# Kernel optimization log

Measured on AMD Instinct MI355X. Metric: run time of the kernel, lower is better.

The kernel has to match this reference:

```python
import jax, jax.numpy as jnp
import numpy as np

B, N = 8, 2048
D_IN, D_FEAT, H, K = 2, 30, 64, 8
D_ATT = D_IN + D_FEAT + H  # 96, per-head attention input dim
ALPHA = 0.2
NEG = -1e9


def setup_inputs() -> dict:
    key = jax.random.key(0)
    ks = jax.random.split(key, 11)
    inputs = jax.random.normal(ks[0], (B, N, D_IN), jnp.float32)
    envs_feat = jax.random.normal(ks[1], (B, N, D_FEAT), jnp.float32)
    state_t = jax.random.normal(ks[2], (B, N, H), jnp.float32)
    conn = jax.random.uniform(ks[3], (N, N)) < 0.05
    conn = conn | jnp.eye(N, dtype=bool)
    bias_mat = jnp.where(conn, 0.0, NEG).astype(jnp.float32)
    # xavier-ish init (gain 1.414)
    def xav(k, shape, fi, fo):
        lim = 1.414 * np.sqrt(6.0 / (fi + fo))
        return jax.random.uniform(k, shape, jnp.float32, -lim, lim)
    W_h = xav(ks[4], (K, D_ATT, H), D_ATT, H)      # stacked per-head W
    a1_h = xav(ks[5], (K, H), H, 1)
    a2_h = xav(ks[6], (K, H), H, 1)
    W_o = xav(ks[7], (K * H, H), K * H, H)
    a1_o = xav(ks[8], (H,), H, 1)
    a2_o = xav(ks[9], (H,), H, 1)
    return {"inputs": inputs, "envs_feat": envs_feat, "state_t": state_t,
            "bias_mat": bias_mat, "W_h": W_h, "a1_h": a1_h, "a2_h": a2_h,
            "W_o": W_o, "a1_o": a1_o, "a2_o": a2_o}


def _gat_multihead(h, bias, W, a1, a2):
    # h: [b,n,d], W: [k,d,h], a1/a2: [k,h], bias: [n,n]
    Wh = jnp.einsum('bnd,kdh->bknh', h, W)
    f1 = jnp.einsum('bknh,kh->bkn', Wh, a1)
    f2 = jnp.einsum('bknh,kh->bkn', Wh, a2)
    e = jax.nn.leaky_relu(f1[:, :, :, None] + f2[:, :, None, :], ALPHA) + bias  # [b,k,n,n]
    att = jax.nn.softmax(e, axis=-1)
    return jnp.einsum('bknm,bkmh->bknh', att, Wh)  # [b,k,n,h]


def _gat_single(h, bias, W, a1, a2):
    # h: [b,n,d], W: [d,h], a1/a2: [h]
    Wh = jnp.einsum('bnd,dh->bnh', h, W)
    f1 = Wh @ a1  # [b,n]
    f2 = Wh @ a2
    e = jax.nn.leaky_relu(f1[:, :, None] + f2[:, None, :], ALPHA) + bias  # [b,n,n]
    att = jax.nn.softmax(e, axis=-1)
    return jnp.einsum('bnm,bmh->bnh', att, Wh)


def reference(inputs, envs_feat, state_t, bias_mat, W_h, a1_h, a2_h, W_o, a1_o, a2_o):
    b, n = inputs.shape[0], inputs.shape[1]
    h = jnp.concatenate([inputs, envs_feat, state_t], axis=2)  # [b,n,D_ATT]
    hp = _gat_multihead(h, bias_mat, W_h, a1_h, a2_h)          # [b,k,n,h]
    h1 = jax.nn.elu(hp)
    h1 = jnp.transpose(h1, (0, 2, 1, 3)).reshape(b, n, -1)     # concat heads: [b,n,k*h]
    out = jax.nn.elu(_gat_single(h1, bias_mat, W_o, a1_o, a2_o))
    return out
```

## Files before the change

### kernel.cpp

```cpp
#include <hip/hip_runtime.h>
#include <hip/hip_bf16.h>
#include <math.h>

#define B   8
#define N   2048
#define DIN 2
#define DF  30
#define HH  64
#define KK  8
#define DATT 96
#define CAP 384
#define CAPL 176
#define ALPHA 0.2f

__device__ __forceinline__ float lrelu(float x) { return x > 0.f ? x : ALPHA * x; }
__device__ __forceinline__ float elu1(float x)  { return x > 0.f ? x : (__expf(x) - 1.f); }
__device__ __forceinline__ unsigned short f2bf(float x) {
    __hip_bfloat16 h = __float2bfloat16(x);
    return *reinterpret_cast<unsigned short*>(&h);
}

__global__ void k_mask(const float* __restrict__ bias, int* __restrict__ cols,
                       int* __restrict__ cnt) {
    int i = blockIdx.x;
    int lane = threadIdx.x;
    int c = 0;
    for (int j0 = 0; j0 < N; j0 += 64) {
        float v = bias[(size_t)i * N + j0 + lane];
        bool conn = v > -1e8f;
        unsigned long long m = __ballot(conn);
        if (conn) {
            int pos = c + __popcll(m & ((1ull << lane) - 1ull));
            if (pos < CAP) cols[i * CAP + pos] = j0 + lane;
        }
        c += __popcll(m);
    }
    if (lane == 0) cnt[i] = c < CAP ? c : CAP;
}

__global__ void k_wh(const float* __restrict__ inp, const float* __restrict__ envs,
                     const float* __restrict__ st,  const float* __restrict__ W_h,
                     const float* __restrict__ a1,  const float* __restrict__ a2,
                     __hip_bfloat16* __restrict__ Whb,
                     float* __restrict__ f1, float* __restrict__ f2) {
    __shared__ float Ws[DATT * HH];
    __shared__ float hs[16 * 98];
    int k = blockIdx.y, b = blockIdx.z;
    int i0 = blockIdx.x * 16;
    int tid = threadIdx.x, lane = tid & 63, w = tid >> 6;
    int g = lane >> 4, sub = lane & 15;
    int r = w * 4 + g;

    const float* Wk = W_h + k * DATT * HH;
    for (int idx = tid * 4; idx < DATT * HH; idx += 1024)
        *(float4*)&Ws[idx] = *(const float4*)&Wk[idx];
    {
        int row = tid >> 4, q = tid & 15;
        float4 v = *(const float4*)&st[(size_t)(b * N + i0 + row) * HH + q * 4];
        float* hb = &hs[row * 98 + DIN + DF + q * 4];
        hb[0] = v.x; hb[1] = v.y; hb[2] = v.z; hb[3] = v.w;
    }
    if (tid < 240) {
        int row = tid / 15, q = tid % 15;
        float2 v = *(const float2*)&envs[(size_t)(b * N + i0 + row) * DF + q * 2];
        float* hb = &hs[row * 98 + DIN + q * 2];
        hb[0] = v.x; hb[1] = v.y;
    }
    if (tid < 32) {
        int row = tid >> 1, q = tid & 1;
        hs[row * 98 + q] = inp[(size_t)(b * N + i0 + row) * DIN + q];
    }
    __syncthreads();

    const float* hb = &hs[r * 98];
    float4 acc = make_float4(0.f, 0.f, 0.f, 0.f);
#pragma unroll
    for (int d = 0; d < DATT; d += 2) {
        float2 hv = *(const float2*)&hb[d];
        float4 w0 = *(const float4*)&Ws[d * HH + sub * 4];
        float4 w1 = *(const float4*)&Ws[(d + 1) * HH + sub * 4];
        acc.x += hv.x * w0.x; acc.y += hv.x * w0.y;
        acc.z += hv.x * w0.z; acc.w += hv.x * w0.w;
        acc.x += hv.y * w1.x; acc.y += hv.y * w1.y;
        acc.z += hv.y * w1.z; acc.w += hv.y * w1.w;
    }
    int i = i0 + r;
    int bkN = (b * KK + k) * N;
    unsigned int lo = (unsigned)f2bf(acc.x) | ((unsigned)f2bf(acc.y) << 16);
    unsigned int hi = (unsigned)f2bf(acc.z) | ((unsigned)f2bf(acc.w) << 16);
    *(uint2*)&Whb[((size_t)bkN + i) * HH + sub * 4] = make_uint2(lo, hi);
    float4 a1v = *(const float4*)&a1[k * HH + sub * 4];
    float4 a2v = *(const float4*)&a2[k * HH + sub * 4];
    float p1 = acc.x * a1v.x + acc.y * a1v.y + acc.z * a1v.z + acc.w * a1v.w;
    float p2 = acc.x * a2v.x + acc.y * a2v.y + acc.z * a2v.z + acc.w * a2v.w;
#pragma unroll
    for (int off = 8; off; off >>= 1) {
        p1 += __shfl_xor(p1, off);
        p2 += __shfl_xor(p2, off);
    }
    if (sub == 0) { f1[bkN + i] = p1; f2[bkN + i] = p2; }
}

__global__ void k_attn(const __hip_bfloat16* __restrict__ Whb, const float* __restrict__ f1,
                       const float* __restrict__ f2, const int* __restrict__ cols,
                       const int* __restrict__ cnt, float* __restrict__ h1) {
    __shared__ float2 sedge[16][CAPL + 2];
    int flat = blockIdx.y * 128 + blockIdx.x;
    int xcd = flat & 7, sq = flat >> 3;
    int bk = (xcd << 3) | (sq >> 7);
    int tile = sq & 127;
    int b = bk >> 3, k = bk & 7;
    int tid = threadIdx.x;
    int lane = tid & 63, w = tid >> 6;
    int g = lane >> 4, sub = lane & 15;
    int r = w * 4 + g;
    int i = tile * 16 + r;

    int c = cnt[i]; if (c > CAPL) c = CAPL;
    float f1i = f1[bk * N + i];
    const int* cl = cols + (size_t)i * CAP;
    const float* f2p = f2 + bk * N;

    float m = -1e30f;
    for (int e = sub; e < c; e += 16) {
        int j = cl[e];
        float sc = lrelu(f1i + f2p[j]);
        sedge[r][e] = make_float2(__int_as_float(j << 7), sc);
        m = fmaxf(m, sc);
    }
#pragma unroll
    for (int off = 8; off; off >>= 1) m = fmaxf(m, __shfl_xor(m, off));

    float Z = 0.f;
    for (int e = sub; e < c; e += 16) {
        float wt = __expf(sedge[r][e].y - m);
        sedge[r][e].y = wt;
        Z += wt;
    }
#pragma unroll
    for (int off = 8; off; off >>= 1) Z += __shfl_xor(Z, off);
    float invZ = 1.f / Z;

    const char* Whp = (const char*)(Whb + (size_t)bk * N * HH);
    int lane8 = sub << 3;
    float4 acc = make_float4(0.f, 0.f, 0.f, 0.f);
    int e = 0;
    for (; e + 4 <= c; e += 4) {
        float2 p0 = sedge[r][e];
        float2 p1 = sedge[r][e + 1];
        float2 p2 = sedge[r][e + 2];
        float2 p3 = sedge[r][e + 3];
        uint2 v0 = *(const uint2*)(Whp + (__float_as_int(p0.x) + lane8));
        uint2 v1 = *(const uint2*)(Whp + (__float_as_int(p1.x) + lane8));
        uint2 v2 = *(const uint2*)(Whp + (__float_as_int(p2.x) + lane8));
        uint2 v3 = *(const uint2*)(Whp + (__float_as_int(p3.x) + lane8));
        acc.x += p0.y * __int_as_float(v0.x << 16);
        acc.y += p0.y * __int_as_float(v0.x & 0xffff0000u);
        acc.z += p0.y * __int_as_float(v0.y << 16);
        acc.w += p0.y * __int_as_float(v0.y & 0xffff0000u);
        acc.x += p1.y * __int_as_float(v1.x << 16);
        acc.y += p1.y * __int_as_float(v1.x & 0xffff0000u);
        acc.z += p1.y * __int_as_float(v1.y << 16);
        acc.w += p1.y * __int_as_float(v1.y & 0xffff0000u);
        acc.x += p2.y * __int_as_float(v2.x << 16);
        acc.y += p2.y * __int_as_float(v2.x & 0xffff0000u);
        acc.z += p2.y * __int_as_float(v2.y << 16);
        acc.w += p2.y * __int_as_float(v2.y & 0xffff0000u);
        acc.x += p3.y * __int_as_float(v3.x << 16);
        acc.y += p3.y * __int_as_float(v3.x & 0xffff0000u);
        acc.z += p3.y * __int_as_float(v3.y << 16);
        acc.w += p3.y * __int_as_float(v3.y & 0xffff0000u);
    }
    for (; e < c; ++e) {
        float2 p0 = sedge[r][e];
        uint2 v0 = *(const uint2*)(Whp + (__float_as_int(p0.x) + lane8));
        acc.x += p0.y * __int_as_float(v0.x << 16);
        acc.y += p0.y * __int_as_float(v0.x & 0xffff0000u);
        acc.z += p0.y * __int_as_float(v0.y << 16);
        acc.w += p0.y * __int_as_float(v0.y & 0xffff0000u);
    }
    float4 o;
    o.x = elu1(acc.x * invZ); o.y = elu1(acc.y * invZ);
    o.z = elu1(acc.z * invZ); o.w = elu1(acc.w * invZ);
    *(float4*)&h1[(size_t)(b * N + i) * (KK * HH) + k * HH + sub * 4] = o;
}

__global__ void k_who(const float* __restrict__ h1, const float* __restrict__ W_o,
                      const float* __restrict__ a1o, const float* __restrict__ a2o,
                      float* __restrict__ Who, float* __restrict__ f1o,
                      float* __restrict__ f2o) {
    __shared__ float Ws[128 * HH];
    int tid = threadIdx.x, lane = tid & 63, w = tid >> 6;
    int g = lane >> 4, sub = lane & 15;
    int row = blockIdx.x * 16 + w * 4 + g;
    const float* hp = h1 + (size_t)row * (KK * HH);
    float4 acc = make_float4(0.f, 0.f, 0.f, 0.f);
    for (int ph = 0; ph < 4; ++ph) {
        __syncthreads();
        for (int idx = tid * 4; idx < 128 * HH; idx += 1024)
            *(float4*)&Ws[idx] = *(const float4*)&W_o[ph * 128 * HH + idx];
        __syncthreads();
#pragma unroll 4
        for (int d0 = 0; d0 < 128; d0 += 4) {
            float4 hv = *(const float4*)(hp + ph * 128 + d0);
#pragma unroll
            for (int dd = 0; dd < 4; ++dd) {
                float hsv = dd == 0 ? hv.x : dd == 1 ? hv.y : dd == 2 ? hv.z : hv.w;
                float4 wv = *(const float4*)&Ws[(d0 + dd) * HH + sub * 4];
                acc.x += hsv * wv.x; acc.y += hsv * wv.y;
                acc.z += hsv * wv.z; acc.w += hsv * wv.w;
            }
        }
    }
    *(float4*)&Who[(size_t)row * HH + sub * 4] = acc;
    float4 a1v = *(const float4*)&a1o[sub * 4];
    float4 a2v = *(const float4*)&a2o[sub * 4];
    float p1 = acc.x * a1v.x + acc.y * a1v.y + acc.z * a1v.z + acc.w * a1v.w;
    float p2 = acc.x * a2v.x + acc.y * a2v.y + acc.z * a2v.z + acc.w * a2v.w;
#pragma unroll
    for (int off = 8; off; off >>= 1) {
        p1 += __shfl_xor(p1, off);
        p2 += __shfl_xor(p2, off);
    }
    if (sub == 0) { f1o[row] = p1; f2o[row] = p2; }
}

__global__ void k_attn2(const float* __restrict__ Who, const float* __restrict__ f1o,
                        const float* __restrict__ f2o, const int* __restrict__ cols,
                        const int* __restrict__ cnt, float* __restrict__ out) {
    __shared__ float2 sedge[16][CAPL + 2];
    int flat = blockIdx.y * 128 + blockIdx.x;
    int b = flat & 7;
    int tile = flat >> 3;
    int tid = threadIdx.x;
    int lane = tid & 63, w = tid >> 6;
    int g = lane >> 4, sub = lane & 15;
    int r = w * 4 + g;
    int i = tile * 16 + r;

    int c = cnt[i]; if (c > CAPL) c = CAPL;
    float f1i = f1o[b * N + i];
    const int* cl = cols + (size_t)i * CAP;
    const float* f2p = f2o + b * N;

    float m = -1e30f;
    for (int e = sub; e < c; e += 16) {
        int j = cl[e];
        float sc = lrelu(f1i + f2p[j]);
        sedge[r][e] = make_float2(__int_as_float(j << 8), sc);
        m = fmaxf(m, sc);
    }
#pragma unroll
    for (int off = 8; off; off >>= 1) m = fmaxf(m, __shfl_xor(m, off));

    float Z = 0.f;
    for (int e = sub; e < c; e += 16) {
        float wt = __expf(sedge[r][e].y - m);
        sedge[r][e].y = wt;
        Z += wt;
    }
#pragma unroll
    for (int off = 8; off; off >>= 1) Z += __shfl_xor(Z, off);
    float invZ = 1.f / Z;

    const char* Wp = (const char*)(Who + (size_t)b * N * HH);
    int lane4 = sub << 4;
    float4 acc = make_float4(0.f, 0.f, 0.f, 0.f);
    int e = 0;
    for (; e + 4 <= c; e += 4) {
        float2 p0 = sedge[r][e];
        float2 p1 = sedge[r][e + 1];
        float2 p2 = sedge[r][e + 2];
        float2 p3 = sedge[r][e + 3];
        float4 v0 = *(const float4*)(Wp + (__float_as_int(p0.x) + lane4));
        float4 v1 = *(const float4*)(Wp + (__float_as_int(p1.x) + lane4));
        float4 v2 = *(const float4*)(Wp + (__float_as_int(p2.x) + lane4));
        float4 v3 = *(const float4*)(Wp + (__float_as_int(p3.x) + lane4));
        acc.x += p0.y * v0.x; acc.y += p0.y * v0.y;
        acc.z += p0.y * v0.z; acc.w += p0.y * v0.w;
        acc.x += p1.y * v1.x; acc.y += p1.y * v1.y;
        acc.z += p1.y * v1.z; acc.w += p1.y * v1.w;
        acc.x += p2.y * v2.x; acc.y += p2.y * v2.y;
        acc.z += p2.y * v2.z; acc.w += p2.y * v2.w;
        acc.x += p3.y * v3.x; acc.y += p3.y * v3.y;
        acc.z += p3.y * v3.z; acc.w += p3.y * v3.w;
    }
    for (; e < c; ++e) {
        float2 p0 = sedge[r][e];
        float4 v0 = *(const float4*)(Wp + (__float_as_int(p0.x) + lane4));
        acc.x += p0.y * v0.x; acc.y += p0.y * v0.y;
        acc.z += p0.y * v0.z; acc.w += p0.y * v0.w;
    }
    float4 o;
    o.x = elu1(acc.x * invZ); o.y = elu1(acc.y * invZ);
    o.z = elu1(acc.z * invZ); o.w = elu1(acc.w * invZ);
    *(float4*)&out[(size_t)(b * N + i) * HH + sub * 4] = o;
}

extern "C" void kernel_launch(void* const* d_in, const int* in_sizes, int n_in,
                              void* d_out, int out_size, void* d_ws, size_t ws_size,
                              hipStream_t stream) {
    const float* inp   = (const float*)d_in[0];
    const float* envs  = (const float*)d_in[1];
    const float* st    = (const float*)d_in[2];
    const float* bias  = (const float*)d_in[3];
    const float* W_h   = (const float*)d_in[4];
    const float* a1_h  = (const float*)d_in[5];
    const float* a2_h  = (const float*)d_in[6];
    const float* W_o   = (const float*)d_in[7];
    const float* a1_o  = (const float*)d_in[8];
    const float* a2_o  = (const float*)d_in[9];
    float* out = (float*)d_out;

    char* ws = (char*)d_ws;
    size_t off = 0;
    __hip_bfloat16* Whb = (__hip_bfloat16*)(ws + off); off += (size_t)B * KK * N * HH * 2;
    float* f1  = (float*)(ws + off); off += (size_t)B * KK * N * 4;
    float* f2  = (float*)(ws + off); off += (size_t)B * KK * N * 4;
    float* h1  = (float*)(ws + off); off += (size_t)B * N * KK * HH * 4;
    float* Who = (float*)(ws + off); off += (size_t)B * N * HH * 4;
    float* f1o = (float*)(ws + off); off += (size_t)B * N * 4;
    float* f2o = (float*)(ws + off); off += (size_t)B * N * 4;
    int*   cols = (int*)(ws + off);  off += (size_t)N * CAP * 4;
    int*   cnt  = (int*)(ws + off);  off += (size_t)N * 4;

    k_mask<<<dim3(N), dim3(64), 0, stream>>>(bias, cols, cnt);
    k_wh<<<dim3(N / 16, KK, B), dim3(256), 0, stream>>>(inp, envs, st, W_h, a1_h, a2_h,
                                                        Whb, f1, f2);
    k_attn<<<dim3(N / 16, B * KK), dim3(256), 0, stream>>>(Whb, f1, f2, cols, cnt, h1);
    k_who<<<dim3(B * N / 16), dim3(256), 0, stream>>>(h1, W_o, a1_o, a2_o, Who, f1o, f2o);
    k_attn2<<<dim3(N / 16, B), dim3(256), 0, stream>>>(Who, f1o, f2o, cols, cnt, out);
}
```

Before: 315.2 us.

## Process all heads per row in one wave with node-major bf16 Wh layout

Wh is now stored node-major as [b,n,k*h] in bf16, and f1/f2 as [b,n,k], so a single 64-lane wave can handle one target row across all 8 heads. Each neighbor gather becomes one contiguous 1 KB load of all heads, and the column list is read once instead of once per head. The second attention kernel likewise switches to one wave per row with a wave-uniform neighbor index. This removes repeated column-list and score work per head and makes the gathers more coalesced. In exchange it lowers parallelism per row and adds shared-memory score tables per wave.

```diff
diff --git a/kernel.cpp b/kernel.cpp
--- a/kernel.cpp
+++ b/kernel.cpp
@@ -19,6 +19,8 @@
     __hip_bfloat16 h = __float2bfloat16(x);
     return *reinterpret_cast<unsigned short*>(&h);
 }
+__device__ __forceinline__ float bflo(unsigned int u) { return __int_as_float(u << 16); }
+__device__ __forceinline__ float bfhi(unsigned int u) { return __int_as_float(u & 0xffff0000u); }
 
 __global__ void k_mask(const float* __restrict__ bias, int* __restrict__ cols,
                        int* __restrict__ cnt) {
@@ -41,8 +43,8 @@
 __global__ void k_wh(const float* __restrict__ inp, const float* __restrict__ envs,
                      const float* __restrict__ st,  const float* __restrict__ W_h,
                      const float* __restrict__ a1,  const float* __restrict__ a2,
-                     __hip_bfloat16* __restrict__ Whb,
-                     float* __restrict__ f1, float* __restrict__ f2) {
+                     unsigned short* __restrict__ Whb,
+                     float* __restrict__ f1n, float* __restrict__ f2n) {
     __shared__ float Ws[DATT * HH];
     __shared__ float hs[16 * 98];
     int k = blockIdx.y, b = blockIdx.z;
@@ -85,10 +87,9 @@
         acc.z += hv.y * w1.z; acc.w += hv.y * w1.w;
     }
     int i = i0 + r;
-    int bkN = (b * KK + k) * N;
     unsigned int lo = (unsigned)f2bf(acc.x) | ((unsigned)f2bf(acc.y) << 16);
     unsigned int hi = (unsigned)f2bf(acc.z) | ((unsigned)f2bf(acc.w) << 16);
-    *(uint2*)&Whb[((size_t)bkN + i) * HH + sub * 4] = make_uint2(lo, hi);
+    *(uint2*)&Whb[((size_t)(b * N + i)) * (KK * HH) + k * HH + sub * 4] = make_uint2(lo, hi);
     float4 a1v = *(const float4*)&a1[k * HH + sub * 4];
     float4 a2v = *(const float4*)&a2[k * HH + sub * 4];
     float p1 = acc.x * a1v.x + acc.y * a1v.y + acc.z * a1v.z + acc.w * a1v.w;
@@ -98,91 +99,76 @@
         p1 += __shfl_xor(p1, off);
         p2 += __shfl_xor(p2, off);
     }
-    if (sub == 0) { f1[bkN + i] = p1; f2[bkN + i] = p2; }
-}
-
-__global__ void k_attn(const __hip_bfloat16* __restrict__ Whb, const float* __restrict__ f1,
-                       const float* __restrict__ f2, const int* __restrict__ cols,
+    if (sub == 0) {
+        f1n[((size_t)(b * N + i)) * KK + k] = p1;
+        f2n[((size_t)(b * N + i)) * KK + k] = p2;
+    }
+}
+
+__global__ void k_attn(const unsigned short* __restrict__ Whb, const float* __restrict__ f1n,
+                       const float* __restrict__ f2n, const int* __restrict__ cols,
                        const int* __restrict__ cnt, float* __restrict__ h1) {
-    __shared__ float2 sedge[16][CAPL + 2];
-    int flat = blockIdx.y * 128 + blockIdx.x;
-    int xcd = flat & 7, sq = flat >> 3;
-    int bk = (xcd << 3) | (sq >> 7);
-    int tile = sq & 127;
-    int b = bk >> 3, k = bk & 7;
-    int tid = threadIdx.x;
-    int lane = tid & 63, w = tid >> 6;
-    int g = lane >> 4, sub = lane & 15;
-    int r = w * 4 + g;
-    int i = tile * 16 + r;
+    __shared__ float sw[4][CAPL + 8][8];
+    __shared__ int   jl[4][CAPL];
+    int flat = blockIdx.y * (N / 4) + blockIdx.x;
+    int b = flat & 7, tile = flat >> 3;
+    int tid = threadIdx.x, lane = tid & 63, w = tid >> 6;
+    int i = tile * 4 + w;
+    int k = lane >> 3, q = lane & 7;
 
     int c = cnt[i]; if (c > CAPL) c = CAPL;
-    float f1i = f1[bk * N + i];
     const int* cl = cols + (size_t)i * CAP;
-    const float* f2p = f2 + bk * N;
-
-    float m = -1e30f;
-    for (int e = sub; e < c; e += 16) {
-        int j = cl[e];
-        float sc = lrelu(f1i + f2p[j]);
-        sedge[r][e] = make_float2(__int_as_float(j << 7), sc);
-        m = fmaxf(m, sc);
-    }
-#pragma unroll
-    for (int off = 8; off; off >>= 1) m = fmaxf(m, __shfl_xor(m, off));
-
-    float Z = 0.f;
-    for (int e = sub; e < c; e += 16) {
-        float wt = __expf(sedge[r][e].y - m);
-        sedge[r][e].y = wt;
-        Z += wt;
-    }
-#pragma unroll
-    for (int off = 8; off; off >>= 1) Z += __shfl_xor(Z, off);
-    float invZ = 1.f / Z;
-
-    const char* Whp = (const char*)(Whb + (size_t)bk * N * HH);
-    int lane8 = sub << 3;
-    float4 acc = make_float4(0.f, 0.f, 0.f, 0.f);
-    int e = 0;
-    for (; e + 4 <= c; e += 4) {
-        float2 p0 = sedge[r][e];
-        float2 p1 = sedge[r][e + 1];
-        float2 p2 = sedge[r][e + 2];
-        float2 p3 = sedge[r][e + 3];
-        uint2 v0 = *(const uint2*)(Whp + (__float_as_int(p0.x) + lane8));
-        uint2 v1 = *(const uint2*)(Whp + (__float_as_int(p1.x) + lane8));
-        uint2 v2 = *(const uint2*)(Whp + (__float_as_int(p2.x) + lane8));
-        uint2 v3 = *(const uint2*)(Whp + (__float_as_int(p3.x) + lane8));
-        acc.x += p0.y * __int_as_float(v0.x << 16);
-        acc.y += p0.y * __int_as_float(v0.x & 0xffff0000u);
-        acc.z += p0.y * __int_as_float(v0.y << 16);
-        acc.w += p0.y * __int_as_float(v0.y & 0xffff0000u);
-        acc.x += p1.y * __int_as_float(v1.x << 16);
-        acc.y += p1.y * __int_as_float(v1.x & 0xffff0000u);
-        acc.z += p1.y * __int_as_float(v1.y << 16);
-        acc.w += p1.y * __int_as_float(v1.y & 0xffff0000u);
-        acc.x += p2.y * __int_as_float(v2.x << 16);
-        acc.y += p2.y * __int_as_float(v2.x & 0xffff0000u);
-        acc.z += p2.y * __int_as_float(v2.y << 16);
-        acc.w += p2.y * __int_as_float(v2.y & 0xffff0000u);
-        acc.x += p3.y * __int_as_float(v3.x << 16);
-        acc.y += p3.y * __int_as_float(v3.x & 0xffff0000u);
-        acc.z += p3.y * __int_as_float(v3.y << 16);
-        acc.w += p3.y * __int_as_float(v3.y & 0xffff0000u);
-    }
-    for (; e < c; ++e) {
-        float2 p0 = sedge[r][e];
-        uint2 v0 = *(const uint2*)(Whp + (__float_as_int(p0.x) + lane8));
-        acc.x += p0.y * __int_as_float(v0.x << 16);
-        acc.y += p0.y * __int_as_float(v0.x & 0xffff0000u);
-        acc.z += p0.y * __int_as_float(v0.y << 16);
-        acc.w += p0.y * __int_as_float(v0.y & 0xffff0000u);
-    }
-    float4 o;
-    o.x = elu1(acc.x * invZ); o.y = elu1(acc.y * invZ);
-    o.z = elu1(acc.z * invZ); o.w = elu1(acc.w * invZ);
-    *(float4*)&h1[(size_t)(b * N + i) * (KK * HH) + k * HH + sub * 4] = o;
+    for (int e = lane; e < c; e += 64) jl[w][e] = cl[e];
+
+    float f1k = f1n[((size_t)(b * N + i)) * KK + k];
+    const float* f2b = f2n + (size_t)b * N * KK;
+
+    float mk = -1e30f;
+    for (int e0 = 0; e0 < c; e0 += 8) {
+        int e = e0 + q;
+        int ee = e < c ? e : c - 1;
+        int j = jl[w][ee];
+        float s = lrelu(f1k + f2b[(size_t)j * KK + k]);
+        if (e >= c) s = -1e30f;
+        sw[w][e][k] = s;
+        mk = fmaxf(mk, s);
+    }
+#pragma unroll
+    for (int off = 4; off; off >>= 1) mk = fmaxf(mk, __shfl_xor(mk, off));
+
+    float Zk = 0.f;
+    for (int e0 = 0; e0 < c; e0 += 8) {
+        int e = e0 + q;
+        float wt = __expf(sw[w][e][k] - mk);
+        sw[w][e][k] = wt;
+        Zk += wt;
+    }
+#pragma unroll
+    for (int off = 4; off; off >>= 1) Zk += __shfl_xor(Zk, off);
+    float invZ = 1.f / Zk;
+
+    const char* Wp = (const char*)Whb + (size_t)b * N * 1024;
+    float4 aL = make_float4(0.f, 0.f, 0.f, 0.f);
+    float4 aH = make_float4(0.f, 0.f, 0.f, 0.f);
+    int lane16 = lane << 4;
+#pragma unroll 8
+    for (int e = 0; e < c; ++e) {
+        int j = __builtin_amdgcn_readfirstlane(jl[w][e]);
+        float wt = sw[w][e][k];
+        uint4 v = *(const uint4*)(Wp + ((size_t)j << 10) + lane16);
+        aL.x += wt * bflo(v.x); aL.y += wt * bfhi(v.x);
+        aL.z += wt * bflo(v.y); aL.w += wt * bfhi(v.y);
+        aH.x += wt * bflo(v.z); aH.y += wt * bfhi(v.z);
+        aH.z += wt * bflo(v.w); aH.w += wt * bfhi(v.w);
+    }
+    float4 o1, o2;
+    o1.x = elu1(aL.x * invZ); o1.y = elu1(aL.y * invZ);
+    o1.z = elu1(aL.z * invZ); o1.w = elu1(aL.w * invZ);
+    o2.x = elu1(aH.x * invZ); o2.y = elu1(aH.y * invZ);
+    o2.z = elu1(aH.z * invZ); o2.w = elu1(aH.w * invZ);
+    float* hp = &h1[((size_t)(b * N + i)) * (KK * HH) + lane * 8];
+    *(float4*)hp = o1;
+    *(float4*)(hp + 4) = o2;
 }
 
 __global__ void k_who(const float* __restrict__ h1, const float* __restrict__ W_o,
@@ -228,73 +214,53 @@
 __global__ void k_attn2(const float* __restrict__ Who, const float* __restrict__ f1o,
                         const float* __restrict__ f2o, const int* __restrict__ cols,
                         const int* __restrict__ cnt, float* __restrict__ out) {
-    __shared__ float2 sedge[16][CAPL + 2];
-    int flat = blockIdx.y * 128 + blockIdx.x;
-    int b = flat & 7;
-    int tile = flat >> 3;
-    int tid = threadIdx.x;
-    int lane = tid & 63, w = tid >> 6;
-    int g = lane >> 4, sub = lane & 15;
-    int r = w * 4 + g;
-    int i = tile * 16 + r;
+    __shared__ float sw[4][CAPL + 64];
+    __shared__ int   jl[4][CAPL];
+    int flat = blockIdx.y * (N / 4) + blockIdx.x;
+    int b = flat & 7, tile = flat >> 3;
+    int tid = threadIdx.x, lane = tid & 63, w = tid >> 6;
+    int i = tile * 4 + w;
 
     int c = cnt[i]; if (c > CAPL) c = CAPL;
+    const int* cl = cols + (size_t)i * CAP;
+    for (int e = lane; e < c; e += 64) jl[w][e] = cl[e];
+
     float f1i = f1o[b * N + i];
-    const int* cl = cols + (size_t)i * CAP;
-    const float* f2p = f2o + b * N;
+    const float* f2p = f2o + (size_t)b * N;
 
     float m = -1e30f;
-    for (int e = sub; e < c; e += 16) {
-        int j = cl[e];
-        float sc = lrelu(f1i + f2p[j]);
-        sedge[r][e] = make_float2(__int_as_float(j << 8), sc);
-        m = fmaxf(m, sc);
-    }
-#pragma unroll
-    for (int off = 8; off; off >>= 1) m = fmaxf(m, __shfl_xor(m, off));
+    for (int e0 = 0; e0 < c; e0 += 64) {
+        int e = e0 + lane;
+        int ee = e < c ? e : c - 1;
+        int j = jl[w][ee];
+        float s = lrelu(f1i + f2p[j]);
+        if (e >= c) s = -1e30f;
+        sw[w][e] = s;
+        m = fmaxf(m, s);
+    }
+#pragma unroll
+    for (int off = 32; off; off >>= 1) m = fmaxf(m, __shfl_xor(m, off));
 
     float Z = 0.f;
-    for (int e = sub; e < c; e += 16) {
-        float wt = __expf(sedge[r][e].y - m);
-        sedge[r][e].y = wt;
+    for (int e0 = 0; e0 < c; e0 += 64) {
+        int e = e0 + lane;
+        float wt = __expf(sw[w][e] - m);
+        sw[w][e] = wt;
         Z += wt;
     }
 #pragma unroll
-    for (int off = 8; off; off >>= 1) Z += __shfl_xor(Z, off);
+    for (int off = 32; off; off >>= 1) Z += __shfl_xor(Z, off);
     float invZ = 1.f / Z;
 
-    const char* Wp = (const char*)(Who + (size_t)b * N * HH);
-    int lane4 = sub << 4;
-    float4 acc = make_float4(0.f, 0.f, 0.f, 0.f);
-    int e = 0;
-    for (; e + 4 <= c; e += 4) {
-        float2 p0 = sedge[r][e];
-        float2 p1 = sedge[r][e + 1];
-        float2 p2 = sedge[r][e + 2];
-        float2 p3 = sedge[r][e + 3];
-        float4 v0 = *(const float4*)(Wp + (__float_as_int(p0.x) + lane4));
-        float4 v1 = *(const float4*)(Wp + (__float_as_int(p1.x) + lane4));
-        float4 v2 = *(const float4*)(Wp + (__float_as_int(p2.x) + lane4));
-        float4 v3 = *(const float4*)(Wp + (__float_as_int(p3.x) + lane4));
-        acc.x += p0.y * v0.x; acc.y += p0.y * v0.y;
-        acc.z += p0.y * v0.z; acc.w += p0.y * v0.w;
-        acc.x += p1.y * v1.x; acc.y += p1.y * v1.y;
-        acc.z += p1.y * v1.z; acc.w += p1.y * v1.w;
-        acc.x += p2.y * v2.x; acc.y += p2.y * v2.y;
-        acc.z += p2.y * v2.z; acc.w += p2.y * v2.w;
-        acc.x += p3.y * v3.x; acc.y += p3.y * v3.y;
-        acc.z += p3.y * v3.z; acc.w += p3.y * v3.w;
-    }
-    for (; e < c; ++e) {
-        float2 p0 = sedge[r][e];
-        float4 v0 = *(const float4*)(Wp + (__float_as_int(p0.x) + lane4));
-        acc.x += p0.y * v0.x; acc.y += p0.y * v0.y;
-        acc.z += p0.y * v0.z; acc.w += p0.y * v0.w;
-    }
-    float4 o;
-    o.x = elu1(acc.x * invZ); o.y = elu1(acc.y * invZ);
-    o.z = elu1(acc.z * invZ); o.w = elu1(acc.w * invZ);
-    *(float4*)&out[(size_t)(b * N + i) * HH + sub * 4] = o;
+    const float* Wp = Who + (size_t)b * N * HH;
+    float acc = 0.f;
+#pragma unroll 8
+    for (int e = 0; e < c; ++e) {
+        int j = __builtin_amdgcn_readfirstlane(jl[w][e]);
+        float wt = sw[w][e];
+        acc += wt * Wp[((size_t)j << 6) + lane];
+    }
+    out[((size_t)(b * N + i)) * HH + lane] = elu1(acc * invZ);
 }
 
 extern "C" void kernel_launch(void* const* d_in, const int* in_sizes, int n_in,
@@ -314,9 +280,9 @@
 
     char* ws = (char*)d_ws;
     size_t off = 0;
-    __hip_bfloat16* Whb = (__hip_bfloat16*)(ws + off); off += (size_t)B * KK * N * HH * 2;
-    float* f1  = (float*)(ws + off); off += (size_t)B * KK * N * 4;
-    float* f2  = (float*)(ws + off); off += (size_t)B * KK * N * 4;
+    unsigned short* Whb = (unsigned short*)(ws + off); off += (size_t)B * N * KK * HH * 2;
+    float* f1n = (float*)(ws + off); off += (size_t)B * N * KK * 4;
+    float* f2n = (float*)(ws + off); off += (size_t)B * N * KK * 4;
     float* h1  = (float*)(ws + off); off += (size_t)B * N * KK * HH * 4;
     float* Who = (float*)(ws + off); off += (size_t)B * N * HH * 4;
     float* f1o = (float*)(ws + off); off += (size_t)B * N * 4;
@@ -326,8 +292,8 @@
 
     k_mask<<<dim3(N), dim3(64), 0, stream>>>(bias, cols, cnt);
     k_wh<<<dim3(N / 16, KK, B), dim3(256), 0, stream>>>(inp, envs, st, W_h, a1_h, a2_h,
-                                                        Whb, f1, f2);
-    k_attn<<<dim3(N / 16, B * KK), dim3(256), 0, stream>>>(Whb, f1, f2, cols, cnt, h1);
+                                                        Whb, f1n, f2n);
+    k_attn<<<dim3(N / 4, B), dim3(256), 0, stream>>>(Whb, f1n, f2n, cols, cnt, h1);
     k_who<<<dim3(B * N / 16), dim3(256), 0, stream>>>(h1, W_o, a1_o, a2_o, Who, f1o, f2o);
-    k_attn2<<<dim3(N / 16, B), dim3(256), 0, stream>>>(Who, f1o, f2o, cols, cnt, out);
-}
+    k_attn2<<<dim3(N / 4, B), dim3(256), 0, stream>>>(Who, f1o, f2o, cols, cnt, out);
+}
```

After: 319.5 us. About the same (+1.4%).
